# Kernel tuning notes

Measured on AMD Instinct MI355X. Metric: run time of the kernel, lower is better.

Reference implementation:

```python
import jax, jax.numpy as jnp
import numpy as np

NEG_INF = -1e9
LRELU_SLOPE = 0.2  # torch GAT default leaky_relu negative slope


def setup_inputs() -> dict:
    key = jax.random.key(0)
    k1, k2, k3, k4, k5 = jax.random.split(key, 5)
    N, F_IN, H, DH = 4096, 1433, 8, 8  # n_nodes, in_features, n_heads, per-head dim (n_hidden=64)
    vert = jax.random.normal(k1, (N, F_IN), dtype=jnp.float32)
    edge = jax.random.randint(k2, (N, N), 0, 2, dtype=jnp.int32)  # dense adjacency mask
    W = jax.random.normal(k3, (F_IN, H * DH), dtype=jnp.float32) * 0.05
    a_l = jax.random.normal(k4, (H, DH), dtype=jnp.float32) * 0.05
    a_r = jax.random.normal(k5, (H, DH), dtype=jnp.float32) * 0.05
    return {"vert": vert, "edge": edge, "W": W, "a_l": a_l, "a_r": a_r}


def reference(vert, edge, W, a_l, a_r):
    # GAT-style edge-affinity layer (is_concat=True) + ELU; dropout is identity (eval mode).
    N = vert.shape[0]
    H, DH = a_l.shape
    g = (vert @ W).reshape(N, H, DH)                      # [N,H,Dh] projected node features
    sl = jnp.einsum('nhd,hd->nh', g, a_l)                 # source-node attention term
    sr = jnp.einsum('nhd,hd->nh', g, a_r)                 # target-node attention term
    e = sl[:, None, :] + sr[None, :, :]                   # [N,N,H]: attn([g_i || g_j])
    e = jnp.where(e >= 0, e, LRELU_SLOPE * e)             # leaky_relu
    mask = (edge != 0)[:, :, None]                        # [N,N,1]
    e = jnp.where(mask, e, NEG_INF)                       # mask non-edges
    a = jax.nn.softmax(e, axis=1)                         # normalize over neighbors j
    out = jnp.einsum('ijh,jhd->ihd', a, g).reshape(N, H * DH)  # aggregate + concat heads
    return jax.nn.elu(out)
```

## Files before the change

### kernel.cpp

```cpp
#include <hip/hip_runtime.h>
#include <hip/hip_bf16.h>

#define NN 4096
#define FIN 1433
#define NH 8
#define DH 8
#define HD 64
#define KP 1472
#define LOG2E 1.44269504f
#define NJS 4
#define NCHK ((NN / NJS) / 128)

typedef unsigned int u32;
typedef unsigned long long u64;
typedef float v4f __attribute__((ext_vector_type(4)));
typedef _Float16 f16;
typedef _Float16 h2 __attribute__((ext_vector_type(2)));
typedef _Float16 f16x8 __attribute__((ext_vector_type(8)));

static __device__ __forceinline__ short f2h16(float f) {
    union { f16 h; short s; } u; u.h = (f16)f; return u.s;
}
static __device__ __forceinline__ h2 u2h2(u32 x) {
    union { u32 u; h2 h; } v; v.u = x; return v.h;
}
static __device__ __forceinline__ u32 h22u(h2 x) {
    union { h2 h; u32 u; } v; v.h = x; return v.u;
}

#if __has_builtin(__builtin_amdgcn_sbfe)
#define SBFE1(x, k) __builtin_amdgcn_sbfe((int)(x), (k), 1)
#else
#define SBFE1(x, k) (((int)((x) << (31 - (k)))) >> 31)
#endif

__global__ __launch_bounds__(256) void k_wprep(const float* __restrict__ W,
                                               short* __restrict__ Wt) {
    __shared__ float Ts[64][65];
    const int c = blockIdx.x;
    const int u = threadIdx.x;
    const int n4 = (u & 15) * 4;
    const int kr = u >> 4;
#pragma unroll
    for (int q = 0; q < 4; ++q) {
        const int kl = kr + q * 16;
        const int kg = c * 64 + kl;
        v4f v = {0.f, 0.f, 0.f, 0.f};
        if (kg < FIN) v = *(const v4f*)&W[(size_t)kg * HD + n4];
        *(v4f*)&Ts[kl][n4] = v;
    }
    __syncthreads();
    const int n = u >> 2;
    const int koff = (u & 3) * 16;
    __align__(16) short tmp[16];
#pragma unroll
    for (int r = 0; r < 16; ++r) tmp[r] = f2h16(Ts[koff + r][n]);
    *(uint4*)&Wt[(size_t)n * KP + c * 64 + koff]     = *(uint4*)&tmp[0];
    *(uint4*)&Wt[(size_t)n * KP + c * 64 + koff + 8] = *(uint4*)&tmp[8];
}

__global__ __launch_bounds__(256, 4) void k_gemm(
    const float* __restrict__ vert, const short* __restrict__ Wt,
    const float* __restrict__ al, const float* __restrict__ ar,
    short* __restrict__ gT, short* __restrict__ eB, short* __restrict__ eD,
    float* __restrict__ Rw)
{
    __shared__ float cacc[4][16][64];

    const int t = threadIdx.x, lane = t & 63, w = t >> 6;
    const int ml = lane & 15, q = lane >> 4;
    const int i0 = blockIdx.x * 16;
    const float* vrow = vert + (size_t)(i0 + ml) * FIN;

    v4f acc[4];
#pragma unroll
    for (int g = 0; g < 4; ++g) acc[g] = (v4f){0.f, 0.f, 0.f, 0.f};

    for (int c = w; c < 45; c += 4) {
        const int k0 = c * 32 + q * 8;
        v4f a0, a1;
        if (k0 + 7 < FIN) {
            a0 = *(const v4f*)&vrow[k0];
            a1 = *(const v4f*)&vrow[k0 + 4];
        } else {
            float tmp[8];
#pragma unroll
            for (int e = 0; e < 8; ++e)
                tmp[e] = (k0 + e < FIN) ? vrow[k0 + e] : 0.f;
            a0 = (v4f){tmp[0], tmp[1], tmp[2], tmp[3]};
            a1 = (v4f){tmp[4], tmp[5], tmp[6], tmp[7]};
        }
        const f16x8 af = {(f16)a0.x, (f16)a0.y, (f16)a0.z, (f16)a0.w,
                          (f16)a1.x, (f16)a1.y, (f16)a1.z, (f16)a1.w};
#pragma unroll
        for (int g = 0; g < 4; ++g) {
            const f16x8 bf = *(const f16x8*)&Wt[(size_t)(g * 16 + ml) * KP + k0];
            acc[g] = __builtin_amdgcn_mfma_f32_16x16x32_f16(af, bf, acc[g], 0, 0, 0);
        }
    }

#pragma unroll
    for (int g = 0; g < 4; ++g)
#pragma unroll
        for (int r = 0; r < 4; ++r)
            cacc[w][q * 4 + r][g * 16 + ml] = acc[g][r];
    __syncthreads();

    const int m = t >> 4, n4 = (t & 15) * 4;
    v4f s = (v4f){0.f, 0.f, 0.f, 0.f};
#pragma unroll
    for (int ww = 0; ww < 4; ++ww) s += *(const v4f*)&cacc[ww][m][n4];

#pragma unroll
    for (int e = 0; e < 4; ++e)
        gT[(size_t)(n4 + e) * NN + i0 + m] = f2h16(s[e]);

    float pl = s.x * al[n4] + s.y * al[n4 + 1] + s.z * al[n4 + 2] + s.w * al[n4 + 3];
    float pr = s.x * ar[n4] + s.y * ar[n4 + 1] + s.z * ar[n4 + 2] + s.w * ar[n4 + 3];
    pl += __shfl_xor(pl, 1, 64);
    pr += __shfl_xor(pr, 1, 64);
    if ((t & 1) == 0) {
        const int h = (t & 15) >> 1;
        const int node = i0 + m;
        eB[h * NN + node] = f2h16(exp2f(pr * LOG2E));
        eD[h * NN + node] = f2h16(exp2f(0.2f * pr * LOG2E));
        Rw[node * NH + h] = exp2f(-0.8f * pl * LOG2E);
    }
}

__global__ __launch_bounds__(256, 4) void k_attn(
    const int* __restrict__ edge, const short* __restrict__ gT,
    const short* __restrict__ eB, const short* __restrict__ eD,
    const float* __restrict__ Rw,
    float* __restrict__ numw, float* __restrict__ denw)
{
    __shared__ __align__(16) short Gt[2][33][136];
    __shared__ __align__(16) short sB[2][4][136];
    __shared__ __align__(16) short sD[2][4][136];
    __shared__ u32 mA[2][32][4];
    __shared__ u32 mB[2][32][4];

    const int t = threadIdx.x, lane = t & 63, w = t >> 6;
    const int ml = lane & 15, quad = lane >> 4;
    const int i0 = blockIdx.x * 32;
    const int hg = blockIdx.y, js = blockIdx.z;
    const int jbase = js * (NN / NJS);
    const int h = hg * 4 + w;

    h2 Ri[2];
#pragma unroll
    for (int it = 0; it < 2; ++it) {
        const f16 rh = (f16)Rw[(i0 + it * 16 + ml) * NH + h];
        Ri[it] = (h2){rh, rh};
    }

    if (t < 136) { Gt[0][32][t] = 0x3C00; Gt[1][32][t] = 0x3C00; }

    const short* gTh = gT + (hg * 32) * NN;
    const short* eBh = eB + (hg * 4) * NN;
    const short* eDh = eD + (hg * 4) * NN;

    const int grow = t >> 3, gseg = (t & 7) * 16;
    const int bh = (t >> 3) & 3, bseg = (t & 7) * 16;

    {
        const int j0 = jbase;
        const uint4 g0 = *(const uint4*)&gTh[grow * NN + j0 + gseg];
        const uint4 g1 = *(const uint4*)&gTh[grow * NN + j0 + gseg + 8];
        *(uint4*)&Gt[0][grow][gseg]     = g0;
        *(uint4*)&Gt[0][grow][gseg + 8] = g1;
        if (t < 32) {
            *(uint4*)&sB[0][bh][bseg]     = *(const uint4*)&eBh[bh * NN + j0 + bseg];
            *(uint4*)&sB[0][bh][bseg + 8] = *(const uint4*)&eBh[bh * NN + j0 + bseg + 8];
        } else if (t < 64) {
            *(uint4*)&sD[0][bh][bseg]     = *(const uint4*)&eDh[bh * NN + j0 + bseg];
            *(uint4*)&sD[0][bh][bseg + 8] = *(const uint4*)&eDh[bh * NN + j0 + bseg + 8];
        }
#pragma unroll
        for (int rr = 0; rr < 8; ++rr) {
            const int row = w * 8 + rr;
            const int2 e2 = *(const int2*)&edge[(i0 + row) * NN + j0 + 2 * lane];
            const u64 bA = __ballot(e2.x != 0);
            const u64 bB = __ballot(e2.y != 0);
            if (lane == 0)  { mA[0][row][0] = (u32)bA;         mB[0][row][0] = (u32)bB; }
            if (lane == 32) { mA[0][row][1] = (u32)(bA >> 32); mB[0][row][1] = (u32)(bB >> 32); }
        }
    }
    __syncthreads();

    v4f acc[2];
    acc[0] = (v4f){0.f, 0.f, 0.f, 0.f};
    acc[1] = (v4f){0.f, 0.f, 0.f, 0.f};

    const int qb4 = quad * 4;
    const int browv = (ml < 8) ? (w * 8 + ml) : 32;

    for (int c = 0; c < NCHK; ++c) {
        const int cb = c & 1, nb = cb ^ 1;
        const bool pf = (c + 1) < NCHK;
        uint4 pg0, pg1, pbd0, pbd1; int2 pe[8];
        if (pf) {
            const int j0 = jbase + (c + 1) * 128;
            pg0 = *(const uint4*)&gTh[grow * NN + j0 + gseg];
            pg1 = *(const uint4*)&gTh[grow * NN + j0 + gseg + 8];
            if (t < 32) {
                pbd0 = *(const uint4*)&eBh[bh * NN + j0 + bseg];
                pbd1 = *(const uint4*)&eBh[bh * NN + j0 + bseg + 8];
            } else if (t < 64) {
                pbd0 = *(const uint4*)&eDh[bh * NN + j0 + bseg];
                pbd1 = *(const uint4*)&eDh[bh * NN + j0 + bseg + 8];
            }
#pragma unroll
            for (int rr = 0; rr < 8; ++rr)
                pe[rr] = *(const int2*)&edge[(i0 + w * 8 + rr) * NN + j0 + 2 * lane];
        }
        uint2 wa[2], wb[2];
#pragma unroll
        for (int it = 0; it < 2; ++it) {
            wa[it] = *(const uint2*)&mA[cb][it * 16 + ml][0];
            wb[it] = *(const uint2*)&mB[cb][it * 16 + ml][0];
        }
#pragma unroll
        for (int s = 0; s < 4; ++s) {
            const uint4 bu = *(const uint4*)&sB[cb][w][s * 32 + quad * 8];
            const uint4 du = *(const uint4*)&sD[cb][w][s * 32 + quad * 8];
            const uint4 gu = *(const uint4*)&Gt[cb][browv][s * 32 + quad * 8];
            union { uint4 u; f16x8 h; } gub; gub.u = gu;
            const f16x8 bfrag = gub.h;
            const int base = ((s & 1) << 4) + qb4;
#pragma unroll
            for (int it = 0; it < 2; ++it) {
                const u32 WA = ((s >> 1) ? wa[it].y : wa[it].x) >> base;
                const u32 WB = ((s >> 1) ? wb[it].y : wb[it].x) >> base;
                u32 aw[4];
#pragma unroll
                for (int k = 0; k < 4; ++k) {
                    const int ea = SBFE1(WA, k);
                    const int eb = SBFE1(WB, k);
                    const u32 m = __builtin_amdgcn_perm((u32)eb, (u32)ea, 0x05040100u);
                    const u32 rd = h22u(Ri[it] * u2h2((&du.x)[k]));
                    u32 pm;
                    asm("v_pk_max_f16 %0, %1, %2" : "=v"(pm) : "v"(rd), "v"((&bu.x)[k]));
                    aw[k] = pm & m;
                }
                union { uint4 u; f16x8 h; } aub;
                aub.u = (uint4){aw[0], aw[1], aw[2], aw[3]};
                acc[it] = __builtin_amdgcn_mfma_f32_16x16x32_f16(aub.h, bfrag, acc[it], 0, 0, 0);
            }
        }
        if (pf) {
            *(uint4*)&Gt[nb][grow][gseg]     = pg0;
            *(uint4*)&Gt[nb][grow][gseg + 8] = pg1;
            if (t < 32) {
                *(uint4*)&sB[nb][bh][bseg]     = pbd0;
                *(uint4*)&sB[nb][bh][bseg + 8] = pbd1;
            } else if (t < 64) {
                *(uint4*)&sD[nb][bh][bseg]     = pbd0;
                *(uint4*)&sD[nb][bh][bseg + 8] = pbd1;
            }
#pragma unroll
            for (int rr = 0; rr < 8; ++rr) {
                const int row = w * 8 + rr;
                const u64 bA = __ballot(pe[rr].x != 0);
                const u64 bB = __ballot(pe[rr].y != 0);
                if (lane == 0)  { mA[nb][row][0] = (u32)bA;         mB[nb][row][0] = (u32)bB; }
                if (lane == 32) { mA[nb][row][1] = (u32)(bA >> 32); mB[nb][row][1] = (u32)(bB >> 32); }
            }
        }
        __syncthreads();
    }

    float* nw = numw + (size_t)js * NN * HD;
    float* dw = denw + (size_t)js * NN * NH;
#pragma unroll
    for (int it = 0; it < 2; ++it) {
        const int ibase = i0 + it * 16 + quad * 4;
#pragma unroll
        for (int r = 0; r < 4; ++r) {
            if (ml < 8)       nw[(ibase + r) * HD + h * 8 + ml] = acc[it][r];
            else if (ml == 8) dw[(ibase + r) * NH + h]          = acc[it][r];
        }
    }
}

__global__ __launch_bounds__(256) void k_comb(
    const float* __restrict__ numw, const float* __restrict__ denw,
    float* __restrict__ out)
{
    const int gid = blockIdx.x * 256 + threadIdx.x;
    const int i = gid >> 6, h = (gid & 63) >> 3;
    float num = 0.f, den = 0.f;
#pragma unroll
    for (int s = 0; s < NJS; ++s) {
        num += numw[s * NN * HD + gid];
        den += denw[s * NN * NH + i * NH + h];
    }
    float x = num / den;
    out[gid] = (x > 0.f) ? x : (__expf(x) - 1.f);
}

extern "C" void kernel_launch(void* const* d_in, const int* in_sizes, int n_in,
                              void* d_out, int out_size, void* d_ws, size_t ws_size,
                              hipStream_t stream) {
    const float* vert = (const float*)d_in[0];
    const int*   edge = (const int*)d_in[1];
    const float* W    = (const float*)d_in[2];
    const float* al   = (const float*)d_in[3];
    const float* ar   = (const float*)d_in[4];
    float* out = (float*)d_out;

    char* ws = (char*)d_ws;
    short* gT   = (short*)ws;
    short* eB   = (short*)(ws + 512 * 1024);
    short* eD   = (short*)(ws + 576 * 1024);
    float* Rw   = (float*)(ws + 640 * 1024);
    short* Wt   = (short*)(ws + 768 * 1024);
    float* numw = (float*)(ws + 1024 * 1024);
    float* denw = (float*)(ws + 5 * 1024 * 1024);

    hipLaunchKernelGGL(k_wprep, dim3(23), dim3(256), 0, stream, W, Wt);
    hipLaunchKernelGGL(k_gemm, dim3(NN / 16), dim3(256), 0, stream,
                       vert, Wt, al, ar, gT, eB, eD, Rw);
    hipLaunchKernelGGL(k_attn, dim3(NN / 32, 2, NJS), dim3(256), 0, stream,
                       edge, gT, eB, eD, Rw, numw, denw);
    hipLaunchKernelGGL(k_comb, dim3(NN * HD / 256), dim3(256), 0, stream,
                       numw, denw, out);
}
```

Baseline: 150.6 us.

## Process all heads per attention block to read edge mask once

Restructures k_attn so each block covers 16 destination rows across all 8 heads instead of 32 rows across 4 heads. The dense int32 edge matrix is then loaded and ballot-packed only once instead of once per head group. One mask is reused for both heads' MFMA operands. In exchange, each block stages twice as many feature and exponent rows in shared memory and the grid doubles in the row dimension.

```diff
diff --git a/kernel.cpp b/kernel.cpp
--- a/kernel.cpp
+++ b/kernel.cpp
@@ -134,51 +134,49 @@
     const float* __restrict__ Rw,
     float* __restrict__ numw, float* __restrict__ denw)
 {
-    __shared__ __align__(16) short Gt[2][33][136];
-    __shared__ __align__(16) short sB[2][4][136];
-    __shared__ __align__(16) short sD[2][4][136];
-    __shared__ u32 mA[2][32][4];
-    __shared__ u32 mB[2][32][4];
+    __shared__ __align__(16) short Gt[2][65][136];
+    __shared__ __align__(16) short sB[2][8][136];
+    __shared__ __align__(16) short sD[2][8][136];
+    __shared__ u32 mA[2][16][4];
+    __shared__ u32 mB[2][16][4];
 
     const int t = threadIdx.x, lane = t & 63, w = t >> 6;
     const int ml = lane & 15, quad = lane >> 4;
-    const int i0 = blockIdx.x * 32;
-    const int hg = blockIdx.y, js = blockIdx.z;
+    const int i0 = blockIdx.x * 16;
+    const int js = blockIdx.y;
     const int jbase = js * (NN / NJS);
-    const int h = hg * 4 + w;
+    const int h0 = w, h1 = w + 4;
 
     h2 Ri[2];
-#pragma unroll
-    for (int it = 0; it < 2; ++it) {
-        const f16 rh = (f16)Rw[(i0 + it * 16 + ml) * NH + h];
-        Ri[it] = (h2){rh, rh};
-    }
-
-    if (t < 136) { Gt[0][32][t] = 0x3C00; Gt[1][32][t] = 0x3C00; }
-
-    const short* gTh = gT + (hg * 32) * NN;
-    const short* eBh = eB + (hg * 4) * NN;
-    const short* eDh = eD + (hg * 4) * NN;
+    {
+        const f16 r0 = (f16)Rw[(i0 + ml) * NH + h0];
+        const f16 r1 = (f16)Rw[(i0 + ml) * NH + h1];
+        Ri[0] = (h2){r0, r0};
+        Ri[1] = (h2){r1, r1};
+    }
+
+    if (t < 136) { Gt[0][64][t] = 0x3C00; Gt[1][64][t] = 0x3C00; }
 
     const int grow = t >> 3, gseg = (t & 7) * 16;
-    const int bh = (t >> 3) & 3, bseg = (t & 7) * 16;
+    const int bh = (t >> 3) & 7, bseg = (t & 7) * 16;
+    const int erow = w * 4;
 
     {
         const int j0 = jbase;
-        const uint4 g0 = *(const uint4*)&gTh[grow * NN + j0 + gseg];
-        const uint4 g1 = *(const uint4*)&gTh[grow * NN + j0 + gseg + 8];
-        *(uint4*)&Gt[0][grow][gseg]     = g0;
-        *(uint4*)&Gt[0][grow][gseg + 8] = g1;
-        if (t < 32) {
-            *(uint4*)&sB[0][bh][bseg]     = *(const uint4*)&eBh[bh * NN + j0 + bseg];
-            *(uint4*)&sB[0][bh][bseg + 8] = *(const uint4*)&eBh[bh * NN + j0 + bseg + 8];
-        } else if (t < 64) {
-            *(uint4*)&sD[0][bh][bseg]     = *(const uint4*)&eDh[bh * NN + j0 + bseg];
-            *(uint4*)&sD[0][bh][bseg + 8] = *(const uint4*)&eDh[bh * NN + j0 + bseg + 8];
-        }
-#pragma unroll
-        for (int rr = 0; rr < 8; ++rr) {
-            const int row = w * 8 + rr;
+        *(uint4*)&Gt[0][grow][gseg]          = *(const uint4*)&gT[grow * NN + j0 + gseg];
+        *(uint4*)&Gt[0][grow][gseg + 8]      = *(const uint4*)&gT[grow * NN + j0 + gseg + 8];
+        *(uint4*)&Gt[0][grow + 32][gseg]     = *(const uint4*)&gT[(grow + 32) * NN + j0 + gseg];
+        *(uint4*)&Gt[0][grow + 32][gseg + 8] = *(const uint4*)&gT[(grow + 32) * NN + j0 + gseg + 8];
+        if (t < 64) {
+            *(uint4*)&sB[0][bh][bseg]     = *(const uint4*)&eB[bh * NN + j0 + bseg];
+            *(uint4*)&sB[0][bh][bseg + 8] = *(const uint4*)&eB[bh * NN + j0 + bseg + 8];
+        } else if (t < 128) {
+            *(uint4*)&sD[0][bh][bseg]     = *(const uint4*)&eD[bh * NN + j0 + bseg];
+            *(uint4*)&sD[0][bh][bseg + 8] = *(const uint4*)&eD[bh * NN + j0 + bseg + 8];
+        }
+#pragma unroll
+        for (int rr = 0; rr < 4; ++rr) {
+            const int row = erow + rr;
             const int2 e2 = *(const int2*)&edge[(i0 + row) * NN + j0 + 2 * lane];
             const u64 bA = __ballot(e2.x != 0);
             const u64 bB = __ballot(e2.y != 0);
@@ -193,74 +191,83 @@
     acc[1] = (v4f){0.f, 0.f, 0.f, 0.f};
 
     const int qb4 = quad * 4;
-    const int browv = (ml < 8) ? (w * 8 + ml) : 32;
+    const int brow0 = (ml < 8) ? (h0 * 8 + ml) : 64;
+    const int brow1 = (ml < 8) ? (h1 * 8 + ml) : 64;
 
     for (int c = 0; c < NCHK; ++c) {
         const int cb = c & 1, nb = cb ^ 1;
         const bool pf = (c + 1) < NCHK;
-        uint4 pg0, pg1, pbd0, pbd1; int2 pe[8];
+        uint4 pg[4], pbd0, pbd1; int2 pe[4];
         if (pf) {
             const int j0 = jbase + (c + 1) * 128;
-            pg0 = *(const uint4*)&gTh[grow * NN + j0 + gseg];
-            pg1 = *(const uint4*)&gTh[grow * NN + j0 + gseg + 8];
-            if (t < 32) {
-                pbd0 = *(const uint4*)&eBh[bh * NN + j0 + bseg];
-                pbd1 = *(const uint4*)&eBh[bh * NN + j0 + bseg + 8];
-            } else if (t < 64) {
-                pbd0 = *(const uint4*)&eDh[bh * NN + j0 + bseg];
-                pbd1 = *(const uint4*)&eDh[bh * NN + j0 + bseg + 8];
-            }
-#pragma unroll
-            for (int rr = 0; rr < 8; ++rr)
-                pe[rr] = *(const int2*)&edge[(i0 + w * 8 + rr) * NN + j0 + 2 * lane];
-        }
-        uint2 wa[2], wb[2];
-#pragma unroll
-        for (int it = 0; it < 2; ++it) {
-            wa[it] = *(const uint2*)&mA[cb][it * 16 + ml][0];
-            wb[it] = *(const uint2*)&mB[cb][it * 16 + ml][0];
-        }
+            pg[0] = *(const uint4*)&gT[grow * NN + j0 + gseg];
+            pg[1] = *(const uint4*)&gT[grow * NN + j0 + gseg + 8];
+            pg[2] = *(const uint4*)&gT[(grow + 32) * NN + j0 + gseg];
+            pg[3] = *(const uint4*)&gT[(grow + 32) * NN + j0 + gseg + 8];
+            if (t < 64) {
+                pbd0 = *(const uint4*)&eB[bh * NN + j0 + bseg];
+                pbd1 = *(const uint4*)&eB[bh * NN + j0 + bseg + 8];
+            } else if (t < 128) {
+                pbd0 = *(const uint4*)&eD[bh * NN + j0 + bseg];
+                pbd1 = *(const uint4*)&eD[bh * NN + j0 + bseg + 8];
+            }
+#pragma unroll
+            for (int rr = 0; rr < 4; ++rr)
+                pe[rr] = *(const int2*)&edge[(i0 + erow + rr) * NN + j0 + 2 * lane];
+        }
+        const uint2 wa = *(const uint2*)&mA[cb][ml][0];
+        const uint2 wb = *(const uint2*)&mB[cb][ml][0];
 #pragma unroll
         for (int s = 0; s < 4; ++s) {
-            const uint4 bu = *(const uint4*)&sB[cb][w][s * 32 + quad * 8];
-            const uint4 du = *(const uint4*)&sD[cb][w][s * 32 + quad * 8];
-            const uint4 gu = *(const uint4*)&Gt[cb][browv][s * 32 + quad * 8];
-            union { uint4 u; f16x8 h; } gub; gub.u = gu;
-            const f16x8 bfrag = gub.h;
+            const uint4 bu0 = *(const uint4*)&sB[cb][h0][s * 32 + quad * 8];
+            const uint4 du0 = *(const uint4*)&sD[cb][h0][s * 32 + quad * 8];
+            const uint4 bu1 = *(const uint4*)&sB[cb][h1][s * 32 + quad * 8];
+            const uint4 du1 = *(const uint4*)&sD[cb][h1][s * 32 + quad * 8];
+            const uint4 gu0 = *(const uint4*)&Gt[cb][brow0][s * 32 + quad * 8];
+            const uint4 gu1 = *(const uint4*)&Gt[cb][brow1][s * 32 + quad * 8];
             const int base = ((s & 1) << 4) + qb4;
-#pragma unroll
-            for (int it = 0; it < 2; ++it) {
-                const u32 WA = ((s >> 1) ? wa[it].y : wa[it].x) >> base;
-                const u32 WB = ((s >> 1) ? wb[it].y : wb[it].x) >> base;
-                u32 aw[4];
-#pragma unroll
-                for (int k = 0; k < 4; ++k) {
-                    const int ea = SBFE1(WA, k);
-                    const int eb = SBFE1(WB, k);
-                    const u32 m = __builtin_amdgcn_perm((u32)eb, (u32)ea, 0x05040100u);
-                    const u32 rd = h22u(Ri[it] * u2h2((&du.x)[k]));
-                    u32 pm;
-                    asm("v_pk_max_f16 %0, %1, %2" : "=v"(pm) : "v"(rd), "v"((&bu.x)[k]));
-                    aw[k] = pm & m;
-                }
-                union { uint4 u; f16x8 h; } aub;
-                aub.u = (uint4){aw[0], aw[1], aw[2], aw[3]};
-                acc[it] = __builtin_amdgcn_mfma_f32_16x16x32_f16(aub.h, bfrag, acc[it], 0, 0, 0);
-            }
+            const u32 WA = ((s >> 1) ? wa.y : wa.x) >> base;
+            const u32 WB = ((s >> 1) ? wb.y : wb.x) >> base;
+            u32 m[4];
+#pragma unroll
+            for (int k = 0; k < 4; ++k) {
+                const int ea = SBFE1(WA, k);
+                const int eb = SBFE1(WB, k);
+                m[k] = __builtin_amdgcn_perm((u32)eb, (u32)ea, 0x05040100u);
+            }
+            u32 aw0[4], aw1[4];
+#pragma unroll
+            for (int k = 0; k < 4; ++k) {
+                const u32 rd0 = h22u(Ri[0] * u2h2((&du0.x)[k]));
+                const u32 rd1 = h22u(Ri[1] * u2h2((&du1.x)[k]));
+                u32 p0, p1;
+                asm("v_pk_max_f16 %0, %1, %2" : "=v"(p0) : "v"(rd0), "v"((&bu0.x)[k]));
+                asm("v_pk_max_f16 %0, %1, %2" : "=v"(p1) : "v"(rd1), "v"((&bu1.x)[k]));
+                aw0[k] = p0 & m[k];
+                aw1[k] = p1 & m[k];
+            }
+            union { uint4 u; f16x8 h; } a0u, a1u, g0u, g1u;
+            a0u.u = (uint4){aw0[0], aw0[1], aw0[2], aw0[3]};
+            a1u.u = (uint4){aw1[0], aw1[1], aw1[2], aw1[3]};
+            g0u.u = gu0; g1u.u = gu1;
+            acc[0] = __builtin_amdgcn_mfma_f32_16x16x32_f16(a0u.h, g0u.h, acc[0], 0, 0, 0);
+            acc[1] = __builtin_amdgcn_mfma_f32_16x16x32_f16(a1u.h, g1u.h, acc[1], 0, 0, 0);
         }
         if (pf) {
-            *(uint4*)&Gt[nb][grow][gseg]     = pg0;
-            *(uint4*)&Gt[nb][grow][gseg + 8] = pg1;
-            if (t < 32) {
+            *(uint4*)&Gt[nb][grow][gseg]          = pg[0];
+            *(uint4*)&Gt[nb][grow][gseg + 8]      = pg[1];
+            *(uint4*)&Gt[nb][grow + 32][gseg]     = pg[2];
+            *(uint4*)&Gt[nb][grow + 32][gseg + 8] = pg[3];
+            if (t < 64) {
                 *(uint4*)&sB[nb][bh][bseg]     = pbd0;
                 *(uint4*)&sB[nb][bh][bseg + 8] = pbd1;
-            } else if (t < 64) {
+            } else if (t < 128) {
                 *(uint4*)&sD[nb][bh][bseg]     = pbd0;
                 *(uint4*)&sD[nb][bh][bseg + 8] = pbd1;
             }
 #pragma unroll
-            for (int rr = 0; rr < 8; ++rr) {
-                const int row = w * 8 + rr;
+            for (int rr = 0; rr < 4; ++rr) {
+                const int row = erow + rr;
                 const u64 bA = __ballot(pe[rr].x != 0);
                 const u64 bB = __ballot(pe[rr].y != 0);
                 if (lane == 0)  { mA[nb][row][0] = (u32)bA;         mB[nb][row][0] = (u32)bB; }
@@ -272,13 +279,14 @@
 
     float* nw = numw + (size_t)js * NN * HD;
     float* dw = denw + (size_t)js * NN * NH;
-#pragma unroll
-    for (int it = 0; it < 2; ++it) {
-        const int ibase = i0 + it * 16 + quad * 4;
+    const int ibase = i0 + quad * 4;
+#pragma unroll
+    for (int hh = 0; hh < 2; ++hh) {
+        const int h = w + hh * 4;
 #pragma unroll
         for (int r = 0; r < 4; ++r) {
-            if (ml < 8)       nw[(ibase + r) * HD + h * 8 + ml] = acc[it][r];
-            else if (ml == 8) dw[(ibase + r) * NH + h]          = acc[it][r];
+            if (ml < 8)       nw[(ibase + r) * HD + h * 8 + ml] = acc[hh][r];
+            else if (ml == 8) dw[(ibase + r) * NH + h]          = acc[hh][r];
         }
     }
 }
@@ -321,7 +329,7 @@
     hipLaunchKernelGGL(k_wprep, dim3(23), dim3(256), 0, stream, W, Wt);
     hipLaunchKernelGGL(k_gemm, dim3(NN / 16), dim3(256), 0, stream,
                        vert, Wt, al, ar, gT, eB, eD, Rw);
-    hipLaunchKernelGGL(k_attn, dim3(NN / 32, 2, NJS), dim3(256), 0, stream,
+    hipLaunchKernelGGL(k_attn, dim3(NN / 16, NJS), dim3(256), 0, stream,
                        edge, gT, eB, eD, Rw, numw, denw);
     hipLaunchKernelGGL(k_comb, dim3(NN * HD / 256), dim3(256), 0, stream,
                        numw, denw, out);
```

After: 149.8 us. Within noise of the previous version (-0.5%).
